# Optimization experiments

Measured on AMD Instinct MI355X. Metric: run time of the kernel, lower is better.

Reference implementation:

```python
import jax, jax.numpy as jnp
import numpy as np

B, N, D = 8, 8192, 64          # batch, input points, point feature dim
NPOINT, NSAMPLE = 1024, 16     # FPS samples S, KNN neighbors K
WN, OUT = 16, 128              # weightnet out channels, output channels
CIN = 3 + D                    # concat(xyz_norm, point feats) = linear in_channel
NEG_SLOPE = 0.1


def setup_inputs() -> dict:
    key = jax.random.key(0)
    ks = jax.random.split(key, 8)
    rn = lambda k, shp, s: jax.random.normal(k, shp, jnp.float32) * s
    return {
        "xyz": rn(ks[0], (B, 3, N), 1.0),
        "points": rn(ks[1], (B, D, N), 1.0),
        "w1": rn(ks[2], (3, 8), 0.5), "b1": jnp.zeros((8,), jnp.float32),
        "w2": rn(ks[3], (8, 8), 0.35), "b2": jnp.zeros((8,), jnp.float32),
        "w3": rn(ks[4], (8, WN), 0.35), "b3": jnp.zeros((WN,), jnp.float32),
        "lin_w": rn(ks[5], (WN * CIN, OUT), 0.03),
        "lin_b": jnp.zeros((OUT,), jnp.float32),
    }


def _fps(xyz):
    """Furthest point sampling. xyz: [B,N,3] -> idx [B,NPOINT] int32."""
    def step(carry, _):
        dist, farthest = carry  # [B,N], [B]
        centroid = jnp.take_along_axis(xyz, farthest[:, None, None], axis=1)  # [B,1,3]
        d = jnp.sum((xyz - centroid) ** 2, axis=-1)  # [B,N]
        dist = jnp.minimum(dist, d)
        return (dist, jnp.argmax(dist, axis=-1).astype(jnp.int32)), farthest
    init = (jnp.full((xyz.shape[0], xyz.shape[1]), 1e10, xyz.dtype),
            jnp.zeros((xyz.shape[0],), jnp.int32))
    _, idxs = jax.lax.scan(step, init, None, length=NPOINT)
    return idxs.T  # [B, NPOINT]


def reference(xyz, points, w1, b1, w2, b2, w3, b3, lin_w, lin_b):
    xyz_t = xyz.transpose(0, 2, 1)       # [B,N,3]
    pts_t = points.transpose(0, 2, 1)    # [B,N,D]

    fps_idx = _fps(xyz_t)                                   # [B,S]
    bidx = jnp.arange(B)[:, None]
    new_xyz = xyz_t[bidx, fps_idx]                          # [B,S,3]

    # KNN: squared distances (same ordering as euclidean cdist)
    sqr = jnp.sum((new_xyz[:, :, None, :] - xyz_t[:, None, :, :]) ** 2, axis=-1)  # [B,S,N]
    _, knn = jax.lax.top_k(-sqr, NSAMPLE)                   # [B,S,K]

    b3i = jnp.arange(B)[:, None, None]
    g_xyz = xyz_t[b3i, knn]                                 # [B,S,K,3]
    g_xyz_norm = g_xyz - new_xyz[:, :, None, :]             # [B,S,K,3]
    g_pts = pts_t[b3i, knn]                                 # [B,S,K,D]
    feat = jnp.concatenate([g_xyz_norm, g_pts], axis=-1)    # [B,S,K,3+D]

    # WeightNet: 1x1 convs == per-neighbor MLP on xyz offsets
    h = jax.nn.relu(g_xyz_norm @ w1 + b1)
    h = jax.nn.relu(h @ w2 + b2)
    wts = jax.nn.relu(h @ w3 + b3)                          # [B,S,K,WN]

    # weighted aggregation over K, then flatten [C, WN]
    agg = jnp.einsum('bskc,bskw->bscw', feat, wts).reshape(B, NPOINT, CIN * WN)
    out = agg @ lin_w + lin_b                               # [B,S,OUT]
    out = jnp.where(out > 0, out, NEG_SLOPE * out)          # LeakyReLU(0.1)

    return new_xyz.transpose(0, 2, 1), out.transpose(0, 2, 1), fps_idx
```

## Files before the change

kernel.cpp:

```cpp
#include <hip/hip_runtime.h>
#include <hip/hip_bf16.h>

#define NPTS   8192
#define NBATCH 8
#define S      1024
#define K      16
#define D      64
#define CIN    67
#define WN     16
#define OUTC   128

#define OUT_MAIN 24576
#define OUT_FPS  1073152

typedef float v2f __attribute__((ext_vector_type(2)));

template <int CTRL, int RM>
__device__ __forceinline__ unsigned long long dpp_max_step(unsigned long long key) {
  int lo = __builtin_amdgcn_update_dpp(0, (int)(unsigned)(key & 0xFFFFFFFFull), CTRL, RM, 0xF, true);
  int hi = __builtin_amdgcn_update_dpp(0, (int)(unsigned)(key >> 32),           CTRL, RM, 0xF, true);
  unsigned long long o = ((unsigned long long)(unsigned)hi << 32) | (unsigned)lo;
  return o > key ? o : key;
}

__global__ __launch_bounds__(512)
void stage0_kernel(const float* __restrict__ xyz, const float* __restrict__ pts,
                   float* __restrict__ newxyz, float* __restrict__ ptt,
                   float* __restrict__ out)
{
#pragma clang fp contract(off)
  __shared__ float s_x[NPTS], s_y[NPTS], s_z[NPTS];
  __shared__ float4 hist[1024];
  __shared__ unsigned long long slots[2][8];

  if (blockIdx.x >= 8) {
    const int bid = blockIdx.x - 8;
    const int b   = bid >> 7;
    const int n0  = (bid & 127) * 64;
    const float* pb = pts + (size_t)b * D * NPTS;
#pragma unroll
    for (int i = 0; i < 8; i++) {
      int s = threadIdx.x + i * 512;
      int nl = s & 63, d = s >> 6;
      s_x[d * 65 + nl] = pb[(size_t)d * NPTS + n0 + nl];
    }
    __syncthreads();
    float* ob = ptt + ((size_t)b * NPTS + n0) * D;
#pragma unroll
    for (int i = 0; i < 8; i++) {
      int s = threadIdx.x + i * 512;
      int dl = s & 63, nl = s >> 6;
      ob[(size_t)nl * D + dl] = s_x[dl * 65 + nl];
    }
    return;
  }

  const int b    = blockIdx.x;
  const int tid  = threadIdx.x;
  const int wave = tid >> 6;
  const int lane = tid & 63;
  const float* xb = xyz + (size_t)b * 3 * NPTS;

  v2f px[8], py[8], pz[8], dist[8];
#pragma unroll
  for (int p = 0; p < 8; p++) {
    int ne = (2 * p) * 512 + tid;
    int no = ne + 512;
    px[p] = (v2f){xb[ne], xb[no]};
    py[p] = (v2f){xb[NPTS + ne], xb[NPTS + no]};
    pz[p] = (v2f){xb[2 * NPTS + ne], xb[2 * NPTS + no]};
    dist[p] = (v2f){1e10f, 1e10f};
    s_x[ne] = px[p].x; s_x[no] = px[p].y;
    s_y[ne] = py[p].x; s_y[no] = py[p].y;
    s_z[ne] = pz[p].x; s_z[no] = pz[p].y;
  }

  int far = 0;
  float cx = xb[0], cy = xb[NPTS], cz = xb[2 * NPTS];

  for (int t = 0; t < 1024; t++) {
    if (tid == (t & 511))
      hist[t] = make_float4(cx, cy, cz, (float)far);

    const v2f c2x = (v2f){cx, cx}, c2y = (v2f){cy, cy}, c2z = (v2f){cz, cz};

    float bd_e = -1.0f, bd_o = -1.0f;
    int   ce   = 0,     co   = 0;
#pragma unroll
    for (int p = 0; p < 8; p++) {
      v2f dx = px[p] - c2x, dy = py[p] - c2y, dz = pz[p] - c2z;
      v2f d  = (dx * dx + dy * dy) + dz * dz;
      float nde = fminf(dist[p].x, d.x);
      float ndo = fminf(dist[p].y, d.y);
      dist[p].x = nde;
      dist[p].y = ndo;
      if (nde > bd_e) { bd_e = nde; ce = 2 * p; }
      if (ndo > bd_o) { bd_o = ndo; co = 2 * p + 1; }
    }

    unsigned long long ke =
        ((unsigned long long)__float_as_uint(bd_e) << 32) | (unsigned)(~(unsigned)(ce * 512 + tid));
    unsigned long long ko =
        ((unsigned long long)__float_as_uint(bd_o) << 32) | (unsigned)(~(unsigned)(co * 512 + tid));
    unsigned long long key = ko > ke ? ko : ke;

    key = dpp_max_step<0x111, 0xF>(key);
    key = dpp_max_step<0x112, 0xF>(key);
    key = dpp_max_step<0x114, 0xF>(key);
    key = dpp_max_step<0x118, 0xF>(key);
    key = dpp_max_step<0x142, 0xA>(key);
    key = dpp_max_step<0x143, 0xC>(key);
    if (lane == 63) slots[t & 1][wave] = key;
    __syncthreads();

    unsigned long long k0 = slots[t & 1][0], k1 = slots[t & 1][1];
    unsigned long long k2 = slots[t & 1][2], k3 = slots[t & 1][3];
    unsigned long long k4 = slots[t & 1][4], k5 = slots[t & 1][5];
    unsigned long long k6 = slots[t & 1][6], k7 = slots[t & 1][7];
    k0 = k1 > k0 ? k1 : k0;
    k2 = k3 > k2 ? k3 : k2;
    k4 = k5 > k4 ? k5 : k4;
    k6 = k7 > k6 ? k7 : k6;
    k0 = k2 > k0 ? k2 : k0;
    k4 = k6 > k4 ? k6 : k4;
    k0 = k4 > k0 ? k4 : k0;
    int gi = (int)(~(unsigned)(k0 & 0xFFFFFFFFull));
    far = gi;
    cx = s_x[gi]; cy = s_y[gi]; cz = s_z[gi];
  }
  __syncthreads();

#pragma unroll
  for (int j = 0; j < 2; j++) {
    int t = j * 512 + tid;
    float4 h = hist[t];
    out[OUT_FPS + b * 1024 + t] = h.w;
    out[b * 3072 + t]           = h.x;
    out[b * 3072 + 1024 + t]    = h.y;
    out[b * 3072 + 2048 + t]    = h.z;
    newxyz[(b * 1024 + t) * 3 + 0] = h.x;
    newxyz[(b * 1024 + t) * 3 + 1] = h.y;
    newxyz[(b * 1024 + t) * 3 + 2] = h.z;
  }
}

__global__ __launch_bounds__(256)
void knn_kernel(const float* __restrict__ xyz, const float* __restrict__ newxyz,
                int* __restrict__ knn)
{
#pragma clang fp contract(off)
  __shared__ unsigned long long s_k[16][16 * 17];
  const int tid   = threadIdx.x;
  const int cl    = tid >> 4;
  const int chunk = tid & 15;
  const int csel  = blockIdx.x * 16 + cl;
  const int b     = csel >> 10;
  const float* xb = xyz + (size_t)b * 3 * NPTS;
  const float cx = newxyz[csel * 3 + 0];
  const float cy = newxyz[csel * 3 + 1];
  const float cz = newxyz[csel * 3 + 2];

  float nd[16]; int ni[16];
#pragma unroll
  for (int k = 0; k < 16; k++) { nd[k] = 3.4e38f; ni[k] = 0x7FFFFFFF; }

  for (int jj = 0; jj < 512; jj++) {
    int j = jj * 16 + chunk;
    float dx = xb[j] - cx, dy = xb[NPTS + j] - cy, dz = xb[2 * NPTS + j] - cz;
    float d  = (dx * dx + dy * dy) + dz * dz;
    float cv = d; int iv = j;
#pragma unroll
    for (int k = 0; k < 16; k++) {
      bool sw = cv < nd[k];
      float tv = nd[k]; int ti = ni[k];
      nd[k] = sw ? cv : tv;  ni[k] = sw ? iv : ti;
      cv    = sw ? tv : cv;  iv    = sw ? ti : iv;
    }
  }
#pragma unroll
  for (int k = 0; k < 16; k++)
    s_k[cl][chunk * 17 + k] =
        ((unsigned long long)__float_as_uint(nd[k]) << 32) | (unsigned)ni[k];
  s_k[cl][chunk * 17 + 16] = ~0ull;
  __syncthreads();

  if (tid < 16) {
    int pos[16];
#pragma unroll
    for (int c = 0; c < 16; c++) pos[c] = 0;
    for (int r = 0; r < 16; r++) {
      unsigned long long bk = ~0ull; int bc = 0;
#pragma unroll
      for (int c = 0; c < 16; c++) {
        unsigned long long kv = s_k[tid][c * 17 + pos[c]];
        if (kv < bk) { bk = kv; bc = c; }
      }
#pragma unroll
      for (int c = 0; c < 16; c++) pos[c] += (c == bc);
      knn[(size_t)(blockIdx.x * 16 + tid) * 16 + r] = (int)(bk & 0xFFFFFFFFull);
    }
  }
}

__global__ __launch_bounds__(256)
void feat_agg_kernel(const float* __restrict__ xyz, const float* __restrict__ newxyz,
                     const float* __restrict__ ptt, const int* __restrict__ knn,
                     const float* __restrict__ w1, const float* __restrict__ b1,
                     const float* __restrict__ w2, const float* __restrict__ b2,
                     const float* __restrict__ w3, const float* __restrict__ b3,
                     float* __restrict__ agg)
{
  const int wv   = threadIdx.x >> 6;
  const int lane = threadIdx.x & 63;
  const int csel = blockIdx.x * 4 + wv;
  const int b    = csel >> 10;

  __shared__ float s_wts[4][16 * 17];
  __shared__ float s_off[4][16 * 3];
  __shared__ int   s_nk[4][16];

  if (lane < 16) {
    int nk = knn[(size_t)csel * 16 + lane];
    s_nk[wv][lane] = nk;
    const float* xb = xyz + (size_t)b * 3 * NPTS;
    float ox = xb[nk]            - newxyz[csel * 3 + 0];
    float oy = xb[NPTS + nk]     - newxyz[csel * 3 + 1];
    float oz = xb[2 * NPTS + nk] - newxyz[csel * 3 + 2];
    s_off[wv][lane * 3 + 0] = ox;
    s_off[wv][lane * 3 + 1] = oy;
    s_off[wv][lane * 3 + 2] = oz;
    float h1[8], h2[8];
#pragma unroll
    for (int j = 0; j < 8; j++)
      h1[j] = fmaxf(0.f, ox * w1[j] + oy * w1[8 + j] + oz * w1[16 + j] + b1[j]);
#pragma unroll
    for (int j = 0; j < 8; j++) {
      float a = b2[j];
#pragma unroll
      for (int i = 0; i < 8; i++) a = fmaf(h1[i], w2[i * 8 + j], a);
      h2[j] = fmaxf(0.f, a);
    }
#pragma unroll
    for (int w = 0; w < 16; w++) {
      float a = b3[w];
#pragma unroll
      for (int i = 0; i < 8; i++) a = fmaf(h2[i], w3[i * 16 + w], a);
      s_wts[wv][lane * 17 + w] = fmaxf(0.f, a);
    }
  }
  __syncthreads();

  float f[16];
#pragma unroll
  for (int k = 0; k < 16; k++) {
    int nk = s_nk[wv][k];
    f[k] = ptt[((size_t)b * NPTS + nk) * D + lane];
  }

  float acc[16];
#pragma unroll
  for (int w = 0; w < 16; w++) acc[w] = 0.f;
#pragma unroll
  for (int k = 0; k < 16; k++) {
#pragma unroll
    for (int w = 0; w < 16; w++)
      acc[w] = fmaf(f[k], s_wts[wv][k * 17 + w], acc[w]);
  }
  float* arow = agg + (size_t)csel * (CIN * WN) + (3 + lane) * 16;
#pragma unroll
  for (int q = 0; q < 4; q++) {
    float4 v = make_float4(acc[4 * q], acc[4 * q + 1], acc[4 * q + 2], acc[4 * q + 3]);
    *(float4*)(arow + 4 * q) = v;
  }

  if (lane < 48) {
    int c = lane >> 4, w = lane & 15;
    float a = 0.f;
#pragma unroll
    for (int k = 0; k < 16; k++)
      a = fmaf(s_off[wv][k * 3 + c], s_wts[wv][k * 17 + w], a);
    agg[(size_t)csel * (CIN * WN) + c * 16 + w] = a;
  }
}

__global__ __launch_bounds__(256)
void gemm_out_kernel(const float* __restrict__ agg, const float* __restrict__ lin_w,
                     const float* __restrict__ lin_b, float* __restrict__ out)
{
  __shared__ float a_t[16 * 68];
  __shared__ float b_t[16 * 64];
  const int tid  = threadIdx.x;
  const int rt   = blockIdx.x >> 1;
  const int ct   = blockIdx.x & 1;
  const int row0 = rt * 64;
  const int c0   = ct * 64;
  const int cg   = tid & 31;
  const int rg   = tid >> 5;

  float acc[8][2] = {};
  for (int kt = 0; kt < 67; kt++) {
    const int k0 = kt * 16;
#pragma unroll
    for (int i = 0; i < 4; i++) {
      int s = tid + i * 256;
      int kk = s & 15, r = s >> 4;
      a_t[kk * 68 + r] = agg[(size_t)(row0 + r) * (CIN * WN) + k0 + kk];
    }
#pragma unroll
    for (int i = 0; i < 4; i++) {
      int s = tid + i * 256;
      int c = s & 63, kk = s >> 6;
      b_t[kk * 64 + c] = lin_w[(size_t)(k0 + kk) * OUTC + c0 + c];
    }
    __syncthreads();
#pragma unroll
    for (int kk = 0; kk < 16; kk++) {
      const float4 a0 = *(const float4*)&a_t[kk * 68 + rg * 8];
      const float4 a1 = *(const float4*)&a_t[kk * 68 + rg * 8 + 4];
      float bv0 = b_t[kk * 64 + cg * 2];
      float bv1 = b_t[kk * 64 + cg * 2 + 1];
      float av[8] = {a0.x, a0.y, a0.z, a0.w, a1.x, a1.y, a1.z, a1.w};
#pragma unroll
      for (int rr = 0; rr < 8; rr++) {
        acc[rr][0] = fmaf(av[rr], bv0, acc[rr][0]);
        acc[rr][1] = fmaf(av[rr], bv1, acc[rr][1]);
      }
    }
    __syncthreads();
  }
#pragma unroll
  for (int rr = 0; rr < 8; rr++) {
#pragma unroll
    for (int cc = 0; cc < 2; cc++) {
      int R = row0 + rg * 8 + rr;
      int C = c0 + cg * 2 + cc;
      float v = acc[rr][cc] + lin_b[C];
      v = v > 0.f ? v : 0.1f * v;
      int bb = R >> 10, ss = R & 1023;
      out[OUT_MAIN + ((size_t)(bb * OUTC + C)) * 1024 + ss] = v;
    }
  }
}

extern "C" void kernel_launch(void* const* d_in, const int* in_sizes, int n_in,
                              void* d_out, int out_size, void* d_ws, size_t ws_size,
                              hipStream_t stream) {
  const float* xyz    = (const float*)d_in[0];
  const float* points = (const float*)d_in[1];
  const float* w1     = (const float*)d_in[2];
  const float* b1     = (const float*)d_in[3];
  const float* w2     = (const float*)d_in[4];
  const float* b2     = (const float*)d_in[5];
  const float* w3     = (const float*)d_in[6];
  const float* b3     = (const float*)d_in[7];
  const float* lin_w  = (const float*)d_in[8];
  const float* lin_b  = (const float*)d_in[9];
  float* out = (float*)d_out;
  char*  ws  = (char*)d_ws;

  float* newxyz = (float*)(ws);
  int*   knn    = (int*)  (ws + 98304);
  float* ptt    = (float*)(ws + 1048576);
  float* agg    = (float*)(ws + 17825792);

  stage0_kernel<<<8 + NBATCH * 128, 512, 0, stream>>>(xyz, points, newxyz, ptt, out);
  knn_kernel<<<512, 256, 0, stream>>>(xyz, newxyz, knn);
  feat_agg_kernel<<<2048, 256, 0, stream>>>(xyz, newxyz, ptt, knn,
                                            w1, b1, w2, b2, w3, b3, agg);
  gemm_out_kernel<<<256, 256, 0, stream>>>(agg, lin_w, lin_b, out);
}
```

Before: 1.365 ms.

## Fuse all stages into a persistent ticketed megakernel with progress flags

Replaces the four kernel launches with a single kernel in which blocks take a ticket and then play the FPS, transpose, KNN, feature-aggregation or GEMM role. FPS publishes its sampled centroids in chunks of 32 through agent-scope release/acquire counters, so KNN, feature and GEMM blocks can start on finished prefixes while the sequential FPS loop is still running. This is meant to hide most of the downstream work behind the FPS critical path and to remove the launch gaps between stages. It adds spin-wait synchronisation and a large shared-memory footprint per block, which limits occupancy. It also depends on ticket order for forward progress. The KNN split is also widened to 32 chunks per centroid.

```diff
diff --git a/kernel.cpp b/kernel.cpp
--- a/kernel.cpp
+++ b/kernel.cpp
@@ -13,7 +13,31 @@
 #define OUT_MAIN 24576
 #define OUT_FPS  1073152
 
+#define T_FPS   0
+#define T_TP    8
+#define T_KNN   1032
+#define T_FEAT  1544
+#define T_GEMM  2568
+#define NBLK    2824
+
 typedef float v2f __attribute__((ext_vector_type(2)));
+
+struct Ctrl {
+  int ticket;
+  int pad0[15];
+  int progress[8];
+  int knn_prefix[8];
+  int tp_done[8];
+  int pad1[8];
+  int tile_done[128];
+};
+
+__device__ __forceinline__ void wait_ge(int* p, int need) {
+  if (threadIdx.x == 0)
+    while (__hip_atomic_load(p, __ATOMIC_ACQUIRE, __HIP_MEMORY_SCOPE_AGENT) < need)
+      __builtin_amdgcn_s_sleep(2);
+  __syncthreads();
+}
 
 template <int CTRL, int RM>
 __device__ __forceinline__ unsigned long long dpp_max_step(unsigned long long key) {
@@ -23,39 +47,16 @@
   return o > key ? o : key;
 }
 
-__global__ __launch_bounds__(512)
-void stage0_kernel(const float* __restrict__ xyz, const float* __restrict__ pts,
-                   float* __restrict__ newxyz, float* __restrict__ ptt,
-                   float* __restrict__ out)
+__device__ void fps_role(int b, const float* __restrict__ xyz, float4* __restrict__ nx4,
+                         float* __restrict__ out, Ctrl* ctrl, void* smem)
 {
 #pragma clang fp contract(off)
-  __shared__ float s_x[NPTS], s_y[NPTS], s_z[NPTS];
-  __shared__ float4 hist[1024];
-  __shared__ unsigned long long slots[2][8];
-
-  if (blockIdx.x >= 8) {
-    const int bid = blockIdx.x - 8;
-    const int b   = bid >> 7;
-    const int n0  = (bid & 127) * 64;
-    const float* pb = pts + (size_t)b * D * NPTS;
-#pragma unroll
-    for (int i = 0; i < 8; i++) {
-      int s = threadIdx.x + i * 512;
-      int nl = s & 63, d = s >> 6;
-      s_x[d * 65 + nl] = pb[(size_t)d * NPTS + n0 + nl];
-    }
-    __syncthreads();
-    float* ob = ptt + ((size_t)b * NPTS + n0) * D;
-#pragma unroll
-    for (int i = 0; i < 8; i++) {
-      int s = threadIdx.x + i * 512;
-      int dl = s & 63, nl = s >> 6;
-      ob[(size_t)nl * D + dl] = s_x[dl * 65 + nl];
-    }
-    return;
-  }
-
-  const int b    = blockIdx.x;
+  float* s_x = (float*)smem;
+  float* s_y = s_x + NPTS;
+  float* s_z = s_y + NPTS;
+  float4* hist = (float4*)((char*)smem + 98304);
+  unsigned long long* slots = (unsigned long long*)((char*)smem + 114688);
+
   const int tid  = threadIdx.x;
   const int wave = tid >> 6;
   const int lane = tid & 63;
@@ -82,6 +83,15 @@
     if (tid == (t & 511))
       hist[t] = make_float4(cx, cy, cz, (float)far);
 
+    if ((t & 31) == 0 && t > 0 && wave == 0 && lane < 32) {
+      int tt = t - 32 + lane;
+      float4 h = hist[tt];
+      nx4[(b << 10) + tt] = h;
+      __threadfence();
+      if (lane == 0)
+        __hip_atomic_store(&ctrl->progress[b], t, __ATOMIC_RELEASE, __HIP_MEMORY_SCOPE_AGENT);
+    }
+
     const v2f c2x = (v2f){cx, cx}, c2y = (v2f){cy, cy}, c2z = (v2f){cz, cz};
 
     float bd_e = -1.0f, bd_o = -1.0f;
@@ -110,13 +120,12 @@
     key = dpp_max_step<0x118, 0xF>(key);
     key = dpp_max_step<0x142, 0xA>(key);
     key = dpp_max_step<0x143, 0xC>(key);
-    if (lane == 63) slots[t & 1][wave] = key;
+    if (lane == 63) slots[(t & 1) * 8 + wave] = key;
     __syncthreads();
 
-    unsigned long long k0 = slots[t & 1][0], k1 = slots[t & 1][1];
-    unsigned long long k2 = slots[t & 1][2], k3 = slots[t & 1][3];
-    unsigned long long k4 = slots[t & 1][4], k5 = slots[t & 1][5];
-    unsigned long long k6 = slots[t & 1][6], k7 = slots[t & 1][7];
+    const unsigned long long* sl = slots + (t & 1) * 8;
+    unsigned long long k0 = sl[0], k1 = sl[1], k2 = sl[2], k3 = sl[3];
+    unsigned long long k4 = sl[4], k5 = sl[5], k6 = sl[6], k7 = sl[7];
     k0 = k1 > k0 ? k1 : k0;
     k2 = k3 > k2 ? k3 : k2;
     k4 = k5 > k4 ? k5 : k4;
@@ -130,6 +139,15 @@
   }
   __syncthreads();
 
+  if (wave == 0 && lane < 32) {
+    int tt = 992 + lane;
+    float4 h = hist[tt];
+    nx4[(b << 10) + tt] = h;
+    __threadfence();
+    if (lane == 0)
+      __hip_atomic_store(&ctrl->progress[b], 1024, __ATOMIC_RELEASE, __HIP_MEMORY_SCOPE_AGENT);
+  }
+
 #pragma unroll
   for (int j = 0; j < 2; j++) {
     int t = j * 512 + tid;
@@ -138,34 +156,61 @@
     out[b * 3072 + t]           = h.x;
     out[b * 3072 + 1024 + t]    = h.y;
     out[b * 3072 + 2048 + t]    = h.z;
-    newxyz[(b * 1024 + t) * 3 + 0] = h.x;
-    newxyz[(b * 1024 + t) * 3 + 1] = h.y;
-    newxyz[(b * 1024 + t) * 3 + 2] = h.z;
-  }
-}
-
-__global__ __launch_bounds__(256)
-void knn_kernel(const float* __restrict__ xyz, const float* __restrict__ newxyz,
-                int* __restrict__ knn)
+  }
+}
+
+__device__ void tp_role(int bid, const float* __restrict__ pts, float* __restrict__ ptt,
+                        Ctrl* ctrl, void* smem)
+{
+  float* tile = (float*)smem;
+  const int b  = bid >> 7;
+  const int n0 = (bid & 127) * 64;
+  const float* pb = pts + (size_t)b * D * NPTS;
+#pragma unroll
+  for (int i = 0; i < 8; i++) {
+    int s = threadIdx.x + i * 512;
+    int nl = s & 63, d = s >> 6;
+    tile[d * 65 + nl] = pb[(size_t)d * NPTS + n0 + nl];
+  }
+  __syncthreads();
+  float* ob = ptt + ((size_t)b * NPTS + n0) * D;
+#pragma unroll
+  for (int i = 0; i < 8; i++) {
+    int s = threadIdx.x + i * 512;
+    int dl = s & 63, nl = s >> 6;
+    ob[(size_t)nl * D + dl] = tile[dl * 65 + nl];
+  }
+  __syncthreads();
+  if (threadIdx.x == 0) {
+    __threadfence();
+    __hip_atomic_fetch_add(&ctrl->tp_done[b], 1, __ATOMIC_RELEASE, __HIP_MEMORY_SCOPE_AGENT);
+  }
+}
+
+__device__ void knn_role(int kidx, const float* __restrict__ xyz, const float4* __restrict__ nx4,
+                         int* __restrict__ knn, Ctrl* ctrl, void* smem)
 {
 #pragma clang fp contract(off)
-  __shared__ unsigned long long s_k[16][16 * 17];
+  unsigned long long (*s_k)[544] = (unsigned long long (*)[544])smem;
   const int tid   = threadIdx.x;
-  const int cl    = tid >> 4;
-  const int chunk = tid & 15;
-  const int csel  = blockIdx.x * 16 + cl;
-  const int b     = csel >> 10;
+  const int cl    = tid >> 5;
+  const int chunk = tid & 31;
+  const int b     = kidx >> 6;
+  const int c0    = (kidx & 63) * 16;
+  const int csel  = (b << 10) + c0 + cl;
+
+  wait_ge(&ctrl->progress[b], c0 + 16);
+
   const float* xb = xyz + (size_t)b * 3 * NPTS;
-  const float cx = newxyz[csel * 3 + 0];
-  const float cy = newxyz[csel * 3 + 1];
-  const float cz = newxyz[csel * 3 + 2];
+  const float4 c4 = nx4[csel];
+  const float cx = c4.x, cy = c4.y, cz = c4.z;
 
   float nd[16]; int ni[16];
 #pragma unroll
   for (int k = 0; k < 16; k++) { nd[k] = 3.4e38f; ni[k] = 0x7FFFFFFF; }
 
-  for (int jj = 0; jj < 512; jj++) {
-    int j = jj * 16 + chunk;
+  for (int jj = 0; jj < 256; jj++) {
+    int j = jj * 32 + chunk;
     float dx = xb[j] - cx, dy = xb[NPTS + j] - cy, dz = xb[2 * NPTS + j] - cz;
     float d  = (dx * dx + dy * dy) + dz * dz;
     float cv = d; int iv = j;
@@ -185,50 +230,63 @@
   __syncthreads();
 
   if (tid < 16) {
-    int pos[16];
-#pragma unroll
-    for (int c = 0; c < 16; c++) pos[c] = 0;
+    int pos[32];
+#pragma unroll
+    for (int c = 0; c < 32; c++) pos[c] = 0;
     for (int r = 0; r < 16; r++) {
       unsigned long long bk = ~0ull; int bc = 0;
 #pragma unroll
-      for (int c = 0; c < 16; c++) {
+      for (int c = 0; c < 32; c++) {
         unsigned long long kv = s_k[tid][c * 17 + pos[c]];
         if (kv < bk) { bk = kv; bc = c; }
       }
 #pragma unroll
-      for (int c = 0; c < 16; c++) pos[c] += (c == bc);
-      knn[(size_t)(blockIdx.x * 16 + tid) * 16 + r] = (int)(bk & 0xFFFFFFFFull);
-    }
-  }
-}
-
-__global__ __launch_bounds__(256)
-void feat_agg_kernel(const float* __restrict__ xyz, const float* __restrict__ newxyz,
-                     const float* __restrict__ ptt, const int* __restrict__ knn,
-                     const float* __restrict__ w1, const float* __restrict__ b1,
-                     const float* __restrict__ w2, const float* __restrict__ b2,
-                     const float* __restrict__ w3, const float* __restrict__ b3,
-                     float* __restrict__ agg)
-{
+      for (int c = 0; c < 32; c++) pos[c] += (c == bc);
+      knn[(size_t)((b << 10) + c0 + tid) * 16 + r] = (int)(bk & 0xFFFFFFFFull);
+    }
+  }
+  __syncthreads();
+  if (tid == 0) {
+    __threadfence();
+    while (__hip_atomic_load(&ctrl->knn_prefix[b], __ATOMIC_ACQUIRE, __HIP_MEMORY_SCOPE_AGENT) < c0)
+      __builtin_amdgcn_s_sleep(2);
+    __hip_atomic_store(&ctrl->knn_prefix[b], c0 + 16, __ATOMIC_RELEASE, __HIP_MEMORY_SCOPE_AGENT);
+  }
+}
+
+__device__ void feat_role(int fidx, const float* __restrict__ xyz, const float4* __restrict__ nx4,
+                          const float* __restrict__ ptt, const int* __restrict__ knn,
+                          const float* __restrict__ w1, const float* __restrict__ b1,
+                          const float* __restrict__ w2, const float* __restrict__ b2,
+                          const float* __restrict__ w3, const float* __restrict__ b3,
+                          float* __restrict__ agg, Ctrl* ctrl, void* smem)
+{
+  float* s_wts = (float*)smem;
+  float* s_off = s_wts + 8 * 272;
+  int*   s_nk  = (int*)(s_off + 8 * 48);
+
+  const int C0 = fidx * 8;
+  const int b  = C0 >> 10;
+  const int c0l = C0 & 1023;
+
+  wait_ge(&ctrl->knn_prefix[b], c0l + 8);
+  wait_ge(&ctrl->tp_done[b], 128);
+
   const int wv   = threadIdx.x >> 6;
   const int lane = threadIdx.x & 63;
-  const int csel = blockIdx.x * 4 + wv;
-  const int b    = csel >> 10;
-
-  __shared__ float s_wts[4][16 * 17];
-  __shared__ float s_off[4][16 * 3];
-  __shared__ int   s_nk[4][16];
+  const int csel = C0 + wv;
 
   if (lane < 16) {
     int nk = knn[(size_t)csel * 16 + lane];
-    s_nk[wv][lane] = nk;
+    s_nk[wv * 16 + lane] = nk;
     const float* xb = xyz + (size_t)b * 3 * NPTS;
-    float ox = xb[nk]            - newxyz[csel * 3 + 0];
-    float oy = xb[NPTS + nk]     - newxyz[csel * 3 + 1];
-    float oz = xb[2 * NPTS + nk] - newxyz[csel * 3 + 2];
-    s_off[wv][lane * 3 + 0] = ox;
-    s_off[wv][lane * 3 + 1] = oy;
-    s_off[wv][lane * 3 + 2] = oz;
+    const float4 c4 = nx4[csel];
+    float ox = xb[nk]            - c4.x;
+    float oy = xb[NPTS + nk]     - c4.y;
+    float oz = xb[2 * NPTS + nk] - c4.z;
+    s_off[wv * 48 + lane * 3 + 0] = ox;
+    s_off[wv * 48 + lane * 3 + 1] = oy;
+    s_off[wv * 48 + lane * 3 + 2] = oz;
     float h1[8], h2[8];
 #pragma unroll
     for (int j = 0; j < 8; j++)
@@ -245,7 +303,7 @@
       float a = b3[w];
 #pragma unroll
       for (int i = 0; i < 8; i++) a = fmaf(h2[i], w3[i * 16 + w], a);
-      s_wts[wv][lane * 17 + w] = fmaxf(0.f, a);
+      s_wts[wv * 272 + lane * 17 + w] = fmaxf(0.f, a);
     }
   }
   __syncthreads();
@@ -253,7 +311,7 @@
   float f[16];
 #pragma unroll
   for (int k = 0; k < 16; k++) {
-    int nk = s_nk[wv][k];
+    int nk = s_nk[wv * 16 + k];
     f[k] = ptt[((size_t)b * NPTS + nk) * D + lane];
   }
 
@@ -264,7 +322,7 @@
   for (int k = 0; k < 16; k++) {
 #pragma unroll
     for (int w = 0; w < 16; w++)
-      acc[w] = fmaf(f[k], s_wts[wv][k * 17 + w], acc[w]);
+      acc[w] = fmaf(f[k], s_wts[wv * 272 + k * 17 + w], acc[w]);
   }
   float* arow = agg + (size_t)csel * (CIN * WN) + (3 + lane) * 16;
 #pragma unroll
@@ -278,50 +336,57 @@
     float a = 0.f;
 #pragma unroll
     for (int k = 0; k < 16; k++)
-      a = fmaf(s_off[wv][k * 3 + c], s_wts[wv][k * 17 + w], a);
+      a = fmaf(s_off[wv * 48 + k * 3 + c], s_wts[wv * 272 + k * 17 + w], a);
     agg[(size_t)csel * (CIN * WN) + c * 16 + w] = a;
   }
-}
-
-__global__ __launch_bounds__(256)
-void gemm_out_kernel(const float* __restrict__ agg, const float* __restrict__ lin_w,
-                     const float* __restrict__ lin_b, float* __restrict__ out)
-{
-  __shared__ float a_t[16 * 68];
-  __shared__ float b_t[16 * 64];
-  const int tid  = threadIdx.x;
-  const int rt   = blockIdx.x >> 1;
-  const int ct   = blockIdx.x & 1;
+  __syncthreads();
+  if (threadIdx.x == 0) {
+    __threadfence();
+    __hip_atomic_fetch_add(&ctrl->tile_done[C0 >> 6], 1, __ATOMIC_RELEASE, __HIP_MEMORY_SCOPE_AGENT);
+  }
+}
+
+__device__ void gemm_role(int gidx, const float* __restrict__ agg, const float* __restrict__ lin_w,
+                          const float* __restrict__ lin_b, float* __restrict__ out,
+                          Ctrl* ctrl, void* smem)
+{
+  float* a_t = (float*)smem;
+  float* b_t = a_t + 16 * 68;
+  const int rt   = gidx >> 1;
+  const int ct   = gidx & 1;
   const int row0 = rt * 64;
   const int c0   = ct * 64;
-  const int cg   = tid & 31;
-  const int rg   = tid >> 5;
-
-  float acc[8][2] = {};
+
+  wait_ge(&ctrl->tile_done[rt], 8);
+
+  const int tid = threadIdx.x;
+  const int cg  = tid & 31;
+  const int rg  = tid >> 5;
+
+  float acc[4][2] = {};
   for (int kt = 0; kt < 67; kt++) {
     const int k0 = kt * 16;
 #pragma unroll
-    for (int i = 0; i < 4; i++) {
-      int s = tid + i * 256;
+    for (int i = 0; i < 2; i++) {
+      int s = tid + i * 512;
       int kk = s & 15, r = s >> 4;
       a_t[kk * 68 + r] = agg[(size_t)(row0 + r) * (CIN * WN) + k0 + kk];
     }
 #pragma unroll
-    for (int i = 0; i < 4; i++) {
-      int s = tid + i * 256;
+    for (int i = 0; i < 2; i++) {
+      int s = tid + i * 512;
       int c = s & 63, kk = s >> 6;
       b_t[kk * 64 + c] = lin_w[(size_t)(k0 + kk) * OUTC + c0 + c];
     }
     __syncthreads();
 #pragma unroll
     for (int kk = 0; kk < 16; kk++) {
-      const float4 a0 = *(const float4*)&a_t[kk * 68 + rg * 8];
-      const float4 a1 = *(const float4*)&a_t[kk * 68 + rg * 8 + 4];
+      const float4 a0 = *(const float4*)&a_t[kk * 68 + rg * 4];
       float bv0 = b_t[kk * 64 + cg * 2];
       float bv1 = b_t[kk * 64 + cg * 2 + 1];
-      float av[8] = {a0.x, a0.y, a0.z, a0.w, a1.x, a1.y, a1.z, a1.w};
-#pragma unroll
-      for (int rr = 0; rr < 8; rr++) {
+      float av[4] = {a0.x, a0.y, a0.z, a0.w};
+#pragma unroll
+      for (int rr = 0; rr < 4; rr++) {
         acc[rr][0] = fmaf(av[rr], bv0, acc[rr][0]);
         acc[rr][1] = fmaf(av[rr], bv1, acc[rr][1]);
       }
@@ -329,10 +394,10 @@
     __syncthreads();
   }
 #pragma unroll
-  for (int rr = 0; rr < 8; rr++) {
+  for (int rr = 0; rr < 4; rr++) {
 #pragma unroll
     for (int cc = 0; cc < 2; cc++) {
-      int R = row0 + rg * 8 + rr;
+      int R = row0 + rg * 4 + rr;
       int C = c0 + cg * 2 + cc;
       float v = acc[rr][cc] + lin_b[C];
       v = v > 0.f ? v : 0.1f * v;
@@ -340,6 +405,35 @@
       out[OUT_MAIN + ((size_t)(bb * OUTC + C)) * 1024 + ss] = v;
     }
   }
+}
+
+__global__ __launch_bounds__(512)
+void mega_kernel(const float* __restrict__ xyz, const float* __restrict__ pts,
+                 const float* __restrict__ w1, const float* __restrict__ b1,
+                 const float* __restrict__ w2, const float* __restrict__ b2,
+                 const float* __restrict__ w3, const float* __restrict__ b3,
+                 const float* __restrict__ lin_w, const float* __restrict__ lin_b,
+                 float* __restrict__ out, float4* __restrict__ nx4,
+                 int* __restrict__ knn, float* __restrict__ ptt,
+                 float* __restrict__ agg, Ctrl* ctrl)
+{
+  __shared__ __align__(16) unsigned long long smem[14400];
+  __shared__ int s_ticket;
+  if (threadIdx.x == 0)
+    s_ticket = __hip_atomic_fetch_add(&ctrl->ticket, 1, __ATOMIC_RELAXED, __HIP_MEMORY_SCOPE_AGENT);
+  __syncthreads();
+  const int tk = s_ticket;
+
+  if (tk < T_TP)
+    fps_role(tk, xyz, nx4, out, ctrl, smem);
+  else if (tk < T_KNN)
+    tp_role(tk - T_TP, pts, ptt, ctrl, smem);
+  else if (tk < T_FEAT)
+    knn_role(tk - T_KNN, xyz, nx4, knn, ctrl, smem);
+  else if (tk < T_GEMM)
+    feat_role(tk - T_FEAT, xyz, nx4, ptt, knn, w1, b1, w2, b2, w3, b3, agg, ctrl, smem);
+  else
+    gemm_role(tk - T_GEMM, agg, lin_w, lin_b, out, ctrl, smem);
 }
 
 extern "C" void kernel_launch(void* const* d_in, const int* in_sizes, int n_in,
@@ -358,14 +452,13 @@
   float* out = (float*)d_out;
   char*  ws  = (char*)d_ws;
 
-  float* newxyz = (float*)(ws);
-  int*   knn    = (int*)  (ws + 98304);
-  float* ptt    = (float*)(ws + 1048576);
-  float* agg    = (float*)(ws + 17825792);
-
-  stage0_kernel<<<8 + NBATCH * 128, 512, 0, stream>>>(xyz, points, newxyz, ptt, out);
-  knn_kernel<<<512, 256, 0, stream>>>(xyz, newxyz, knn);
-  feat_agg_kernel<<<2048, 256, 0, stream>>>(xyz, newxyz, ptt, knn,
-                                            w1, b1, w2, b2, w3, b3, agg);
-  gemm_out_kernel<<<256, 256, 0, stream>>>(agg, lin_w, lin_b, out);
-}
+  float4* nx4  = (float4*)(ws);
+  int*    knn  = (int*)   (ws + 131072);
+  Ctrl*   ctrl = (Ctrl*)  (ws + 655360);
+  float*  ptt  = (float*) (ws + 1048576);
+  float*  agg  = (float*) (ws + 17825792);
+
+  hipMemsetAsync(ctrl, 0, 4096, stream);
+  mega_kernel<<<NBLK, 512, 0, stream>>>(xyz, points, w1, b1, w2, b2, w3, b3,
+                                        lin_w, lin_b, out, nx4, knn, ptt, agg, ctrl);
+}
```

New measurement: 1.543 ms. 13.1% more time.
